# Kernel optimization log

Hardware: AMD Instinct MI355X
Metric: run time of the kernel (lower is better)

Reference implementation:

```python
import jax, jax.numpy as jnp
import numpy as np

B, T, C = 512, 256, 384
HS = 64


def setup_inputs() -> dict:
    key = jax.random.key(0)
    k1, k2, k3, k4 = jax.random.split(key, 4)
    x = jax.random.normal(k1, (B, T, C), dtype=jnp.float32)
    Wk = jax.random.normal(k2, (HS, C), dtype=jnp.float32) * (1.0 / np.sqrt(C))
    Wq = jax.random.normal(k3, (HS, C), dtype=jnp.float32) * (1.0 / np.sqrt(C))
    Wv = jax.random.normal(k4, (HS, C), dtype=jnp.float32) * (1.0 / np.sqrt(C))
    return {"x": x, "Wk": Wk, "Wq": Wq, "Wv": Wv}


def reference(x, Wk, Wq, Wv):
    # x: [B,T,C]; weights: [HS,C] (torch Linear layout, no bias)
    Bv, Tv, Cv = x.shape
    k = jnp.einsum('btc,hc->bth', x, Wk)  # [B,T,HS]
    q = jnp.einsum('btc,hc->bth', x, Wq)
    v = jnp.einsum('btc,hc->bth', x, Wv)
    # scale uses C (n_embd), faithful to source
    wei = jnp.einsum('bth,bsh->bts', q, k) * (Cv ** -0.5)  # [B,T,T]
    causal = jnp.tril(jnp.ones((Tv, Tv), dtype=bool))
    wei = jnp.where(causal, wei, -jnp.inf)
    wei = jax.nn.softmax(wei, axis=-1)
    # dropout is identity in eval mode
    out = jnp.einsum('bts,bsh->bth', wei, v)  # [B,T,HS]
    return out
```

## Files before the change

kernel.cpp:

```cpp
#include <hip/hip_runtime.h>

#define NB 512
#define NT 256
#define NC 384
#define NH 64

typedef __bf16 bf16x8 __attribute__((ext_vector_type(8)));
typedef float f32x4 __attribute__((ext_vector_type(4)));
typedef float f32x16 __attribute__((ext_vector_type(16)));
typedef unsigned int u32;
typedef unsigned int u32x4 __attribute__((ext_vector_type(4)));
typedef unsigned short u16;

__device__ __forceinline__ u16 f2bf(float x) {
  u32 u = __builtin_bit_cast(u32, x);
  u32 r = (u + 0x7fffu + ((u >> 16) & 1u)) >> 16;
  return (u16)r;
}
__device__ __forceinline__ u32 pkbf(float lo, float hi) {
  u32 r;
  asm("v_cvt_pk_bf16_f32 %0, %1, %2" : "=v"(r) : "v"(lo), "v"(hi));
  return r;
}
__device__ __forceinline__ void pl32swap(u32& a, u32& b) {
  asm volatile("v_permlane32_swap_b32 %0, %1" : "+v"(a), "+v"(b));
}

__global__ __launch_bounds__(256) void wconv_k(const float* __restrict__ wk,
                                               const float* __restrict__ wq,
                                               const float* __restrict__ wv,
                                               u16* __restrict__ wb) {
  int i = blockIdx.x * 256 + threadIdx.x;
  if (i >= 192 * NC) return;
  int row = i / NC, c = i - row * NC;
  int g = c >> 3, jj = c & 7;
  int lgr = g ^ (row & 7);
  int cl = lgr * 8 + jj;
  int chunk = cl >> 5, lgj = (cl >> 3) & 3, j = cl & 7;
  int phys = chunk * 32 + (j < 4 ? lgj * 4 + j : 16 + lgj * 4 + (j - 4));
  const float* s = (row < 64) ? wk : ((row < 128) ? wq : wv);
  wb[i] = f2bf(s[(row & 63) * NC + phys]);
}

__global__ __launch_bounds__(1024) void fused_k(const float* __restrict__ x,
                                                const u16* __restrict__ wb,
                                                float* __restrict__ out) {
  __shared__ __align__(16) char smem[147456];
  u16* Wl = (u16*)smem;
  const int tid = threadIdx.x;
  const int lane = tid & 63, w = tid >> 6;
  const int l15 = lane & 15, lg = lane >> 4;
  const int l31 = lane & 31, gl = lane >> 5;
  const int s7 = l15 & 7;
  const size_t m0 = (size_t)blockIdx.x * 256;

  const float* xp = x + (m0 + (size_t)(w * 16 + l15)) * NC + lg * 4;
  const int rot = (w + (int)blockIdx.x) % 12;

  float4 pX[4], pY[4];
#pragma unroll
  for (int s = 0; s < 4; ++s) {
    int kc = rot + s; if (kc >= 12) kc -= 12;
    pX[s] = *(const float4*)(xp + kc * 32);
    pY[s] = *(const float4*)(xp + kc * 32 + 16);
  }
#pragma unroll
  for (int i = 0; i < 9; ++i) {
    int idx = tid + i * 1024;
    *(uint4*)((char*)Wl + idx * 16) = *(const uint4*)((const char*)wb + idx * 16);
  }
  __syncthreads();

  f32x4 acc[12];
#pragma unroll
  for (int nt = 0; nt < 12; ++nt) {
    f32x4 z = {};
    acc[nt] = z;
  }
#pragma unroll
  for (int kk = 0; kk < 12; ++kk) {
    const int st = kk & 3;
    int kc = rot + kk; if (kc >= 12) kc -= 12;
    u32x4 av = {pkbf(pX[st].x, pX[st].y), pkbf(pX[st].z, pX[st].w),
                pkbf(pY[st].x, pY[st].y), pkbf(pY[st].z, pY[st].w)};
    bf16x8 afrag = __builtin_bit_cast(bf16x8, av);
    if (kk < 8) {
      int kc4 = rot + kk + 4; if (kc4 >= 12) kc4 -= 12;
      pX[st] = *(const float4*)(xp + kc4 * 32);
      pY[st] = *(const float4*)(xp + kc4 * 32 + 16);
    }
    const int xorp = ((kc * 4 + lg) ^ s7) << 4;
#pragma unroll
    for (int nt = 0; nt < 12; ++nt) {
      int brow = nt * 16 + l15;
      bf16x8 b = *(const bf16x8*)((const char*)Wl + brow * 768 + xorp);
      acc[nt] = __builtin_amdgcn_mfma_f32_16x16x32_bf16(afrag, b, acc[nt], 0, 0, 0);
    }
  }
  __syncthreads();

  char* Kb = smem;
  char* Vb = smem + 32768;
  char* Qb = smem + 65536;
  float* mlb = (float*)(smem + 98304);
  float* aob = (float*)(smem + 102400);
#pragma unroll
  for (int nt = 0; nt < 12; ++nt) {
#pragma unroll
    for (int r = 0; r < 4; ++r) {
      int s = w * 16 + lg * 4 + r;
      u16 v = f2bf(acc[nt][r]);
      if (nt < 4) {
        int h = nt * 16 + l15;
        *(u16*)(Kb + s * 128 + ((h * 2) ^ ((s & 7) << 4))) = v;
      } else if (nt < 8) {
        int h = (nt - 4) * 16 + l15;
        *(u16*)(Qb + s * 128 + ((h * 2) ^ ((s & 7) << 4))) = v;
      } else {
        int h = (nt - 8) * 16 + l15;
        *(u16*)(Vb + h * 512 + ((s * 2) ^ ((h & 7) << 4))) = v;
      }
    }
  }
  __syncthreads();

  const float cexp = 0.05103103630798287f * 1.4426950408889634f;
  const bool lo = (w < 8);
  const int qt = lo ? w : (15 - w);
  const int t0 = qt * 32;
  const int f1 = lo ? ((qt + 1 < 4) ? qt + 1 : 4) : (qt + 1);
  const int f0 = lo ? 0 : 4;
  const int tq = t0 + l31;

  f32x16 sf[4];
#pragma unroll
  for (int fi = 0; fi < 4; ++fi) {
    int f = f0 + fi;
    if (f < f1) {
      f32x16 z = {};
      sf[fi] = z;
#pragma unroll
      for (int kk = 0; kk < 4; ++kk) {
        int arow = f * 32 + l31;
        bf16x8 a = *(const bf16x8*)(Kb + arow * 128 +
                                    ((kk * 32 + gl * 16) ^ ((arow & 7) << 4)));
        bf16x8 bq = *(const bf16x8*)(Qb + tq * 128 +
                                     ((kk * 32 + gl * 16) ^ ((tq & 7) << 4)));
        sf[fi] = __builtin_amdgcn_mfma_f32_32x32x16_bf16(a, bq, sf[fi], 0, 0, 0);
      }
    }
  }

  float pm = -INFINITY;
#pragma unroll
  for (int fi = 0; fi < 4; ++fi) {
    int f = f0 + fi;
    if (f < f1) {
      if (f < qt) {
#pragma unroll
        for (int r = 0; r < 16; ++r) pm = fmaxf(pm, sf[fi][r]);
      } else {
#pragma unroll
        for (int r = 0; r < 16; ++r) {
          int sloc = (r & 3) + 8 * (r >> 2) + 4 * gl;
          pm = fmaxf(pm, (sloc <= l31) ? sf[fi][r] : -INFINITY);
        }
      }
    }
  }
  pm = fmaxf(pm, __shfl_xor(pm, 32));
  if (gl == 0) mlb[(qt * 2 + (lo ? 0 : 1)) * 32 + l31] = pm;
  __syncthreads();
  float m = fmaxf(pm, mlb[(qt * 2 + (lo ? 1 : 0)) * 32 + l31]);

  float ls = 0.0f;
#pragma unroll
  for (int fi = 0; fi < 4; ++fi) {
    int f = f0 + fi;
    if (f < f1) {
#pragma unroll
      for (int r = 0; r < 16; ++r) {
        float e = exp2f((sf[fi][r] - m) * cexp);
        if (f == qt) {
          int sloc = (r & 3) + 8 * (r >> 2) + 4 * gl;
          e = (sloc <= l31) ? e : 0.0f;
        }
        sf[fi][r] = e;
        ls += e;
      }
    }
  }
  ls += __shfl_xor(ls, 32);
  if (gl == 0) mlb[512 + (qt * 2 + (lo ? 0 : 1)) * 32 + l31] = ls;
  __syncthreads();
  float lsum = ls + mlb[512 + (qt * 2 + (lo ? 1 : 0)) * 32 + l31];

  f32x16 ao0 = {}, ao1 = {};
#pragma unroll
  for (int fi = 0; fi < 4; ++fi) {
    int f = f0 + fi;
    if (f < f1) {
      u32 a0 = pkbf(sf[fi][0], sf[fi][1]);
      u32 a1 = pkbf(sf[fi][2], sf[fi][3]);
      u32 b0 = pkbf(sf[fi][4], sf[fi][5]);
      u32 b1 = pkbf(sf[fi][6], sf[fi][7]);
      pl32swap(a0, b0);
      pl32swap(a1, b1);
      u32x4 te = {a0, a1, b0, b1};
      bf16x8 bpe = __builtin_bit_cast(bf16x8, te);
      u32 c0 = pkbf(sf[fi][8], sf[fi][9]);
      u32 c1 = pkbf(sf[fi][10], sf[fi][11]);
      u32 d0 = pkbf(sf[fi][12], sf[fi][13]);
      u32 d1 = pkbf(sf[fi][14], sf[fi][15]);
      pl32swap(c0, d0);
      pl32swap(c1, d1);
      u32x4 to = {c0, c1, d0, d1};
      bf16x8 bpo = __builtin_bit_cast(bf16x8, to);

      int se = (f * 32 + gl * 8) * 2;
      int so = se + 32;
      bf16x8 av0e = *(const bf16x8*)(Vb + l31 * 512 + (se ^ ((l31 & 7) << 4)));
      bf16x8 av1e = *(const bf16x8*)(Vb + (32 + l31) * 512 + (se ^ ((l31 & 7) << 4)));
      ao0 = __builtin_amdgcn_mfma_f32_32x32x16_bf16(av0e, bpe, ao0, 0, 0, 0);
      ao1 = __builtin_amdgcn_mfma_f32_32x32x16_bf16(av1e, bpe, ao1, 0, 0, 0);
      bf16x8 av0o = *(const bf16x8*)(Vb + l31 * 512 + (so ^ ((l31 & 7) << 4)));
      bf16x8 av1o = *(const bf16x8*)(Vb + (32 + l31) * 512 + (so ^ ((l31 & 7) << 4)));
      ao0 = __builtin_amdgcn_mfma_f32_32x32x16_bf16(av0o, bpo, ao0, 0, 0, 0);
      ao1 = __builtin_amdgcn_mfma_f32_32x32x16_bf16(av1o, bpo, ao1, 0, 0, 0);
    }
  }

  if (!lo) {
#pragma unroll
    for (int r = 0; r < 16; ++r) {
      int hrow = (r & 3) + 8 * (r >> 2) + 4 * gl;
      aob[qt * 1024 + hrow * 32 + l31] = ao0[r];
    }
  }
  __syncthreads();
  if (lo) {
#pragma unroll
    for (int r = 0; r < 16; ++r) {
      int hrow = (r & 3) + 8 * (r >> 2) + 4 * gl;
      ao0[r] += aob[qt * 1024 + hrow * 32 + l31];
    }
  }
  __syncthreads();
  if (!lo) {
#pragma unroll
    for (int r = 0; r < 16; ++r) {
      int hrow = (r & 3) + 8 * (r >> 2) + 4 * gl;
      aob[qt * 1024 + hrow * 32 + l31] = ao1[r];
    }
  }
  __syncthreads();
  if (lo) {
    float rl = 1.0f / lsum;
    float* ob = out + (m0 + t0 + l31) * NH;
#pragma unroll
    for (int g = 0; g < 4; ++g) {
      float4 v0, v1;
#pragma unroll
      for (int j = 0; j < 4; ++j) {
        int r = 4 * g + j;
        int hrow = (r & 3) + 8 * (r >> 2) + 4 * gl;
        float a1c = ao1[r] + aob[qt * 1024 + hrow * 32 + l31];
        ((float*)&v0)[j] = ao0[r] * rl;
        ((float*)&v1)[j] = a1c * rl;
      }
      *(float4*)(ob + 8 * g + 4 * gl) = v0;
      *(float4*)(ob + 32 + 8 * g + 4 * gl) = v1;
    }
  }
}

extern "C" void kernel_launch(void* const* d_in, const int* in_sizes, int n_in,
                              void* d_out, int out_size, void* d_ws, size_t ws_size,
                              hipStream_t stream) {
  const float* x = (const float*)d_in[0];
  const float* wk = (const float*)d_in[1];
  const float* wq = (const float*)d_in[2];
  const float* wv = (const float*)d_in[3];
  float* out = (float*)d_out;

  u16* wb = (u16*)d_ws;

  wconv_k<<<288, 256, 0, stream>>>(wk, wq, wv, wb);
  fused_k<<<512, 1024, 0, stream>>>(x, wb, out);
}
```

Before: 67.47 us.

## Process two batches per block and prefetch next batch's x during projection

Each block now handles two batch elements in sequence instead of one, halving the grid to 256 blocks. While the first batch's projection runs, the block starts loading the next batch's x rows into registers, overlapping global loads with compute. The weights are reloaded into shared memory for each batch because the attention stage overwrites them. The risk is that 256 blocks underfill the 256 CUs and the two batches in a block run serially, trading parallelism for overlap.

New measurement: 227.1 us. +236.6%, slower.

```diff
diff --git a/kernel.cpp b/kernel.cpp
--- a/kernel.cpp
+++ b/kernel.cpp
@@ -52,224 +52,241 @@
   const int l15 = lane & 15, lg = lane >> 4;
   const int l31 = lane & 31, gl = lane >> 5;
   const int s7 = l15 & 7;
-  const size_t m0 = (size_t)blockIdx.x * 256;
-
-  const float* xp = x + (m0 + (size_t)(w * 16 + l15)) * NC + lg * 4;
-  const int rot = (w + (int)blockIdx.x) % 12;
+  const int b0 = (int)blockIdx.x * 2;
 
   float4 pX[4], pY[4];
-#pragma unroll
-  for (int s = 0; s < 4; ++s) {
-    int kc = rot + s; if (kc >= 12) kc -= 12;
-    pX[s] = *(const float4*)(xp + kc * 32);
-    pY[s] = *(const float4*)(xp + kc * 32 + 16);
+  {
+    const float* xp = x + ((size_t)b0 * 256 + w * 16 + l15) * NC + lg * 4;
+    const int rot = (w + b0) % 12;
+#pragma unroll
+    for (int s = 0; s < 4; ++s) {
+      int kc = rot + s; if (kc >= 12) kc -= 12;
+      pX[s] = *(const float4*)(xp + kc * 32);
+      pY[s] = *(const float4*)(xp + kc * 32 + 16);
+    }
   }
-#pragma unroll
-  for (int i = 0; i < 9; ++i) {
-    int idx = tid + i * 1024;
-    *(uint4*)((char*)Wl + idx * 16) = *(const uint4*)((const char*)wb + idx * 16);
-  }
-  __syncthreads();
-
-  f32x4 acc[12];
-#pragma unroll
-  for (int nt = 0; nt < 12; ++nt) {
-    f32x4 z = {};
-    acc[nt] = z;
-  }
-#pragma unroll
-  for (int kk = 0; kk < 12; ++kk) {
-    const int st = kk & 3;
-    int kc = rot + kk; if (kc >= 12) kc -= 12;
-    u32x4 av = {pkbf(pX[st].x, pX[st].y), pkbf(pX[st].z, pX[st].w),
-                pkbf(pY[st].x, pY[st].y), pkbf(pY[st].z, pY[st].w)};
-    bf16x8 afrag = __builtin_bit_cast(bf16x8, av);
-    if (kk < 8) {
-      int kc4 = rot + kk + 4; if (kc4 >= 12) kc4 -= 12;
-      pX[st] = *(const float4*)(xp + kc4 * 32);
-      pY[st] = *(const float4*)(xp + kc4 * 32 + 16);
-    }
-    const int xorp = ((kc * 4 + lg) ^ s7) << 4;
+
+#pragma unroll 1
+  for (int bt = 0; bt < 2; ++bt) {
+    const int b = b0 + bt;
+    const size_t m0 = (size_t)b * 256;
+    const float* xp = x + (m0 + (size_t)(w * 16 + l15)) * NC + lg * 4;
+    const int rot = (w + b) % 12;
+    const int rotn = (w + b + 1) % 12;
+
+    __syncthreads();
+#pragma unroll
+    for (int i = 0; i < 9; ++i) {
+      int idx = tid + i * 1024;
+      *(uint4*)((char*)Wl + idx * 16) = *(const uint4*)((const char*)wb + idx * 16);
+    }
+    __syncthreads();
+
+    f32x4 acc[12];
 #pragma unroll
     for (int nt = 0; nt < 12; ++nt) {
-      int brow = nt * 16 + l15;
-      bf16x8 b = *(const bf16x8*)((const char*)Wl + brow * 768 + xorp);
-      acc[nt] = __builtin_amdgcn_mfma_f32_16x16x32_bf16(afrag, b, acc[nt], 0, 0, 0);
-    }
-  }
-  __syncthreads();
-
-  char* Kb = smem;
-  char* Vb = smem + 32768;
-  char* Qb = smem + 65536;
-  float* mlb = (float*)(smem + 98304);
-  float* aob = (float*)(smem + 102400);
-#pragma unroll
-  for (int nt = 0; nt < 12; ++nt) {
-#pragma unroll
-    for (int r = 0; r < 4; ++r) {
-      int s = w * 16 + lg * 4 + r;
-      u16 v = f2bf(acc[nt][r]);
-      if (nt < 4) {
-        int h = nt * 16 + l15;
-        *(u16*)(Kb + s * 128 + ((h * 2) ^ ((s & 7) << 4))) = v;
-      } else if (nt < 8) {
-        int h = (nt - 4) * 16 + l15;
-        *(u16*)(Qb + s * 128 + ((h * 2) ^ ((s & 7) << 4))) = v;
-      } else {
-        int h = (nt - 8) * 16 + l15;
-        *(u16*)(Vb + h * 512 + ((s * 2) ^ ((h & 7) << 4))) = v;
-      }
-    }
-  }
-  __syncthreads();
-
-  const float cexp = 0.05103103630798287f * 1.4426950408889634f;
-  const bool lo = (w < 8);
-  const int qt = lo ? w : (15 - w);
-  const int t0 = qt * 32;
-  const int f1 = lo ? ((qt + 1 < 4) ? qt + 1 : 4) : (qt + 1);
-  const int f0 = lo ? 0 : 4;
-  const int tq = t0 + l31;
-
-  f32x16 sf[4];
-#pragma unroll
-  for (int fi = 0; fi < 4; ++fi) {
-    int f = f0 + fi;
-    if (f < f1) {
-      f32x16 z = {};
-      sf[fi] = z;
-#pragma unroll
-      for (int kk = 0; kk < 4; ++kk) {
-        int arow = f * 32 + l31;
-        bf16x8 a = *(const bf16x8*)(Kb + arow * 128 +
-                                    ((kk * 32 + gl * 16) ^ ((arow & 7) << 4)));
-        bf16x8 bq = *(const bf16x8*)(Qb + tq * 128 +
-                                     ((kk * 32 + gl * 16) ^ ((tq & 7) << 4)));
-        sf[fi] = __builtin_amdgcn_mfma_f32_32x32x16_bf16(a, bq, sf[fi], 0, 0, 0);
-      }
-    }
-  }
-
-  float pm = -INFINITY;
-#pragma unroll
-  for (int fi = 0; fi < 4; ++fi) {
-    int f = f0 + fi;
-    if (f < f1) {
-      if (f < qt) {
-#pragma unroll
-        for (int r = 0; r < 16; ++r) pm = fmaxf(pm, sf[fi][r]);
-      } else {
+      f32x4 z = {};
+      acc[nt] = z;
+    }
+#pragma unroll
+    for (int kk = 0; kk < 12; ++kk) {
+      const int st = kk & 3;
+      int kc = rot + kk; if (kc >= 12) kc -= 12;
+      u32x4 av = {pkbf(pX[st].x, pX[st].y), pkbf(pX[st].z, pX[st].w),
+                  pkbf(pY[st].x, pY[st].y), pkbf(pY[st].z, pY[st].w)};
+      bf16x8 afrag = __builtin_bit_cast(bf16x8, av);
+      if (kk < 8) {
+        int kc4 = rot + kk + 4; if (kc4 >= 12) kc4 -= 12;
+        pX[st] = *(const float4*)(xp + kc4 * 32);
+        pY[st] = *(const float4*)(xp + kc4 * 32 + 16);
+      } else if (bt == 0) {
+        int kc2 = rotn + kk - 8; if (kc2 >= 12) kc2 -= 12;
+        const float* xpn = xp + 256 * NC;
+        pX[st] = *(const float4*)(xpn + kc2 * 32);
+        pY[st] = *(const float4*)(xpn + kc2 * 32 + 16);
+      }
+      const int xorp = ((kc * 4 + lg) ^ s7) << 4;
+#pragma unroll
+      for (int nt = 0; nt < 12; ++nt) {
+        int brow = nt * 16 + l15;
+        bf16x8 bfr = *(const bf16x8*)((const char*)Wl + brow * 768 + xorp);
+        acc[nt] = __builtin_amdgcn_mfma_f32_16x16x32_bf16(afrag, bfr, acc[nt], 0, 0, 0);
+      }
+    }
+    __syncthreads();
+
+    char* Kb = smem;
+    char* Vb = smem + 32768;
+    char* Qb = smem + 65536;
+    float* mlb = (float*)(smem + 98304);
+    float* aob = (float*)(smem + 102400);
+#pragma unroll
+    for (int nt = 0; nt < 12; ++nt) {
+#pragma unroll
+      for (int r = 0; r < 4; ++r) {
+        int s = w * 16 + lg * 4 + r;
+        u16 v = f2bf(acc[nt][r]);
+        if (nt < 4) {
+          int h = nt * 16 + l15;
+          *(u16*)(Kb + s * 128 + ((h * 2) ^ ((s & 7) << 4))) = v;
+        } else if (nt < 8) {
+          int h = (nt - 4) * 16 + l15;
+          *(u16*)(Qb + s * 128 + ((h * 2) ^ ((s & 7) << 4))) = v;
+        } else {
+          int h = (nt - 8) * 16 + l15;
+          *(u16*)(Vb + h * 512 + ((s * 2) ^ ((h & 7) << 4))) = v;
+        }
+      }
+    }
+    __syncthreads();
+
+    const float cexp = 0.05103103630798287f * 1.4426950408889634f;
+    const bool lo = (w < 8);
+    const int qt = lo ? w : (15 - w);
+    const int t0 = qt * 32;
+    const int f1 = lo ? ((qt + 1 < 4) ? qt + 1 : 4) : (qt + 1);
+    const int f0 = lo ? 0 : 4;
+    const int tq = t0 + l31;
+
+    f32x16 sf[4];
+#pragma unroll
+    for (int fi = 0; fi < 4; ++fi) {
+      int f = f0 + fi;
+      if (f < f1) {
+        f32x16 z = {};
+        sf[fi] = z;
+#pragma unroll
+        for (int kk = 0; kk < 4; ++kk) {
+          int arow = f * 32 + l31;
+          bf16x8 a = *(const bf16x8*)(Kb + arow * 128 +
+                                      ((kk * 32 + gl * 16) ^ ((arow & 7) << 4)));
+          bf16x8 bq = *(const bf16x8*)(Qb + tq * 128 +
+                                       ((kk * 32 + gl * 16) ^ ((tq & 7) << 4)));
+          sf[fi] = __builtin_amdgcn_mfma_f32_32x32x16_bf16(a, bq, sf[fi], 0, 0, 0);
+        }
+      }
+    }
+
+    float pm = -INFINITY;
+#pragma unroll
+    for (int fi = 0; fi < 4; ++fi) {
+      int f = f0 + fi;
+      if (f < f1) {
+        if (f < qt) {
+#pragma unroll
+          for (int r = 0; r < 16; ++r) pm = fmaxf(pm, sf[fi][r]);
+        } else {
+#pragma unroll
+          for (int r = 0; r < 16; ++r) {
+            int sloc = (r & 3) + 8 * (r >> 2) + 4 * gl;
+            pm = fmaxf(pm, (sloc <= l31) ? sf[fi][r] : -INFINITY);
+          }
+        }
+      }
+    }
+    pm = fmaxf(pm, __shfl_xor(pm, 32));
+    if (gl == 0) mlb[(qt * 2 + (lo ? 0 : 1)) * 32 + l31] = pm;
+    __syncthreads();
+    float m = fmaxf(pm, mlb[(qt * 2 + (lo ? 1 : 0)) * 32 + l31]);
+
+    float ls = 0.0f;
+#pragma unroll
+    for (int fi = 0; fi < 4; ++fi) {
+      int f = f0 + fi;
+      if (f < f1) {
 #pragma unroll
         for (int r = 0; r < 16; ++r) {
-          int sloc = (r & 3) + 8 * (r >> 2) + 4 * gl;
-          pm = fmaxf(pm, (sloc <= l31) ? sf[fi][r] : -INFINITY);
-        }
-      }
-    }
-  }
-  pm = fmaxf(pm, __shfl_xor(pm, 32));
-  if (gl == 0) mlb[(qt * 2 + (lo ? 0 : 1)) * 32 + l31] = pm;
-  __syncthreads();
-  float m = fmaxf(pm, mlb[(qt * 2 + (lo ? 1 : 0)) * 32 + l31]);
-
-  float ls = 0.0f;
-#pragma unroll
-  for (int fi = 0; fi < 4; ++fi) {
-    int f = f0 + fi;
-    if (f < f1) {
+          float e = exp2f((sf[fi][r] - m) * cexp);
+          if (f == qt) {
+            int sloc = (r & 3) + 8 * (r >> 2) + 4 * gl;
+            e = (sloc <= l31) ? e : 0.0f;
+          }
+          sf[fi][r] = e;
+          ls += e;
+        }
+      }
+    }
+    ls += __shfl_xor(ls, 32);
+    if (gl == 0) mlb[512 + (qt * 2 + (lo ? 0 : 1)) * 32 + l31] = ls;
+    __syncthreads();
+    float lsum = ls + mlb[512 + (qt * 2 + (lo ? 1 : 0)) * 32 + l31];
+
+    f32x16 ao0 = {}, ao1 = {};
+#pragma unroll
+    for (int fi = 0; fi < 4; ++fi) {
+      int f = f0 + fi;
+      if (f < f1) {
+        u32 a0 = pkbf(sf[fi][0], sf[fi][1]);
+        u32 a1 = pkbf(sf[fi][2], sf[fi][3]);
+        u32 e0 = pkbf(sf[fi][4], sf[fi][5]);
+        u32 e1 = pkbf(sf[fi][6], sf[fi][7]);
+        pl32swap(a0, e0);
+        pl32swap(a1, e1);
+        u32x4 te = {a0, a1, e0, e1};
+        bf16x8 bpe = __builtin_bit_cast(bf16x8, te);
+        u32 c0 = pkbf(sf[fi][8], sf[fi][9]);
+        u32 c1 = pkbf(sf[fi][10], sf[fi][11]);
+        u32 d0 = pkbf(sf[fi][12], sf[fi][13]);
+        u32 d1 = pkbf(sf[fi][14], sf[fi][15]);
+        pl32swap(c0, d0);
+        pl32swap(c1, d1);
+        u32x4 to = {c0, c1, d0, d1};
+        bf16x8 bpo = __builtin_bit_cast(bf16x8, to);
+
+        int se = (f * 32 + gl * 8) * 2;
+        int so = se + 32;
+        bf16x8 av0e = *(const bf16x8*)(Vb + l31 * 512 + (se ^ ((l31 & 7) << 4)));
+        bf16x8 av1e = *(const bf16x8*)(Vb + (32 + l31) * 512 + (se ^ ((l31 & 7) << 4)));
+        ao0 = __builtin_amdgcn_mfma_f32_32x32x16_bf16(av0e, bpe, ao0, 0, 0, 0);
+        ao1 = __builtin_amdgcn_mfma_f32_32x32x16_bf16(av1e, bpe, ao1, 0, 0, 0);
+        bf16x8 av0o = *(const bf16x8*)(Vb + l31 * 512 + (so ^ ((l31 & 7) << 4)));
+        bf16x8 av1o = *(const bf16x8*)(Vb + (32 + l31) * 512 + (so ^ ((l31 & 7) << 4)));
+        ao0 = __builtin_amdgcn_mfma_f32_32x32x16_bf16(av0o, bpo, ao0, 0, 0, 0);
+        ao1 = __builtin_amdgcn_mfma_f32_32x32x16_bf16(av1o, bpo, ao1, 0, 0, 0);
+      }
+    }
+
+    if (!lo) {
 #pragma unroll
       for (int r = 0; r < 16; ++r) {
-        float e = exp2f((sf[fi][r] - m) * cexp);
-        if (f == qt) {
-          int sloc = (r & 3) + 8 * (r >> 2) + 4 * gl;
-          e = (sloc <= l31) ? e : 0.0f;
-        }
-        sf[fi][r] = e;
-        ls += e;
-      }
-    }
-  }
-  ls += __shfl_xor(ls, 32);
-  if (gl == 0) mlb[512 + (qt * 2 + (lo ? 0 : 1)) * 32 + l31] = ls;
-  __syncthreads();
-  float lsum = ls + mlb[512 + (qt * 2 + (lo ? 1 : 0)) * 32 + l31];
-
-  f32x16 ao0 = {}, ao1 = {};
-#pragma unroll
-  for (int fi = 0; fi < 4; ++fi) {
-    int f = f0 + fi;
-    if (f < f1) {
-      u32 a0 = pkbf(sf[fi][0], sf[fi][1]);
-      u32 a1 = pkbf(sf[fi][2], sf[fi][3]);
-      u32 b0 = pkbf(sf[fi][4], sf[fi][5]);
-      u32 b1 = pkbf(sf[fi][6], sf[fi][7]);
-      pl32swap(a0, b0);
-      pl32swap(a1, b1);
-      u32x4 te = {a0, a1, b0, b1};
-      bf16x8 bpe = __builtin_bit_cast(bf16x8, te);
-      u32 c0 = pkbf(sf[fi][8], sf[fi][9]);
-      u32 c1 = pkbf(sf[fi][10], sf[fi][11]);
-      u32 d0 = pkbf(sf[fi][12], sf[fi][13]);
-      u32 d1 = pkbf(sf[fi][14], sf[fi][15]);
-      pl32swap(c0, d0);
-      pl32swap(c1, d1);
-      u32x4 to = {c0, c1, d0, d1};
-      bf16x8 bpo = __builtin_bit_cast(bf16x8, to);
-
-      int se = (f * 32 + gl * 8) * 2;
-      int so = se + 32;
-      bf16x8 av0e = *(const bf16x8*)(Vb + l31 * 512 + (se ^ ((l31 & 7) << 4)));
-      bf16x8 av1e = *(const bf16x8*)(Vb + (32 + l31) * 512 + (se ^ ((l31 & 7) << 4)));
-      ao0 = __builtin_amdgcn_mfma_f32_32x32x16_bf16(av0e, bpe, ao0, 0, 0, 0);
-      ao1 = __builtin_amdgcn_mfma_f32_32x32x16_bf16(av1e, bpe, ao1, 0, 0, 0);
-      bf16x8 av0o = *(const bf16x8*)(Vb + l31 * 512 + (so ^ ((l31 & 7) << 4)));
-      bf16x8 av1o = *(const bf16x8*)(Vb + (32 + l31) * 512 + (so ^ ((l31 & 7) << 4)));
-      ao0 = __builtin_amdgcn_mfma_f32_32x32x16_bf16(av0o, bpo, ao0, 0, 0, 0);
-      ao1 = __builtin_amdgcn_mfma_f32_32x32x16_bf16(av1o, bpo, ao1, 0, 0, 0);
-    }
-  }
-
-  if (!lo) {
-#pragma unroll
-    for (int r = 0; r < 16; ++r) {
-      int hrow = (r & 3) + 8 * (r >> 2) + 4 * gl;
-      aob[qt * 1024 + hrow * 32 + l31] = ao0[r];
-    }
-  }
-  __syncthreads();
-  if (lo) {
-#pragma unroll
-    for (int r = 0; r < 16; ++r) {
-      int hrow = (r & 3) + 8 * (r >> 2) + 4 * gl;
-      ao0[r] += aob[qt * 1024 + hrow * 32 + l31];
-    }
-  }
-  __syncthreads();
-  if (!lo) {
-#pragma unroll
-    for (int r = 0; r < 16; ++r) {
-      int hrow = (r & 3) + 8 * (r >> 2) + 4 * gl;
-      aob[qt * 1024 + hrow * 32 + l31] = ao1[r];
-    }
-  }
-  __syncthreads();
-  if (lo) {
-    float rl = 1.0f / lsum;
-    float* ob = out + (m0 + t0 + l31) * NH;
-#pragma unroll
-    for (int g = 0; g < 4; ++g) {
-      float4 v0, v1;
-#pragma unroll
-      for (int j = 0; j < 4; ++j) {
-        int r = 4 * g + j;
         int hrow = (r & 3) + 8 * (r >> 2) + 4 * gl;
-        float a1c = ao1[r] + aob[qt * 1024 + hrow * 32 + l31];
-        ((float*)&v0)[j] = ao0[r] * rl;
-        ((float*)&v1)[j] = a1c * rl;
-      }
-      *(float4*)(ob + 8 * g + 4 * gl) = v0;
-      *(float4*)(ob + 32 + 8 * g + 4 * gl) = v1;
+        aob[qt * 1024 + hrow * 32 + l31] = ao0[r];
+      }
+    }
+    __syncthreads();
+    if (lo) {
+#pragma unroll
+      for (int r = 0; r < 16; ++r) {
+        int hrow = (r & 3) + 8 * (r >> 2) + 4 * gl;
+        ao0[r] += aob[qt * 1024 + hrow * 32 + l31];
+      }
+    }
+    __syncthreads();
+    if (!lo) {
+#pragma unroll
+      for (int r = 0; r < 16; ++r) {
+        int hrow = (r & 3) + 8 * (r >> 2) + 4 * gl;
+        aob[qt * 1024 + hrow * 32 + l31] = ao1[r];
+      }
+    }
+    __syncthreads();
+    if (lo) {
+      float rl = 1.0f / lsum;
+      float* ob = out + (m0 + t0 + l31) * NH;
+#pragma unroll
+      for (int g = 0; g < 4; ++g) {
+        float4 v0, v1;
+#pragma unroll
+        for (int j = 0; j < 4; ++j) {
+          int r = 4 * g + j;
+          int hrow = (r & 3) + 8 * (r >> 2) + 4 * gl;
+          float a1c = ao1[r] + aob[qt * 1024 + hrow * 32 + l31];
+          ((float*)&v0)[j] = ao0[r] * rl;
+          ((float*)&v1)[j] = a1c * rl;
+        }
+        *(float4*)(ob + 8 * g + 4 * gl) = v0;
+        *(float4*)(ob + 32 + 8 * g + 4 * gl) = v1;
+      }
     }
   }
 }
@@ -286,5 +303,5 @@
   u16* wb = (u16*)d_ws;
 
   wconv_k<<<288, 256, 0, stream>>>(wk, wq, wv, wb);
-  fused_k<<<512, 1024, 0, stream>>>(x, wb, out);
-}
+  fused_k<<<256, 1024, 0, stream>>>(x, wb, out);
+}
```
